# Performance work log

Hardware: AMD Instinct MI355X
Metric: run time of the kernel (lower is better)

Reference implementation:

```python
import jax, jax.numpy as jnp
import numpy as np

B, N, RIN, ROUT, DEMB, FIN, FE, E, ITERS = 64, 128, 32, 64, 64, 64, 16, 65536, 3
NTOT = B * N


def gnn(x, edge_index, edge_feat, Ws, Wm, We, b):
    # edge-conditioned message passing: [NTOT, Fin] -> [NTOT, Fout]
    src, dst = edge_index[0], edge_index[1]
    msg = jax.nn.relu(x[src] @ Wm + edge_feat @ We)          # [E, Fout]
    agg = jax.ops.segment_sum(msg, dst, num_segments=x.shape[0])
    return jax.nn.relu(x @ Ws + agg + b)


def setup_inputs() -> dict:
    key = jax.random.key(0)
    ks = jax.random.split(key, 20)
    s = 0.1
    return {
        "x_r": jax.random.normal(ks[0], (NTOT, FIN), jnp.float32),
        "edge_index_r": jax.random.randint(ks[1], (2, E), 0, NTOT),
        "edge_feat_r": jax.random.normal(ks[2], (E, FE), jnp.float32),
        "x_p": jax.random.normal(ks[3], (NTOT, FIN), jnp.float32),
        "edge_index_p": jax.random.randint(ks[4], (2, E), 0, NTOT),
        "edge_feat_p": jax.random.normal(ks[5], (E, FE), jnp.float32),
        "r_mask": jnp.ones((B, N), dtype=bool),
        "p_mask": jnp.ones((B, N), dtype=bool),
        # gnn_1 params (FIN -> DEMB)
        "g1_Ws": jax.random.normal(ks[6], (FIN, DEMB)) * s,
        "g1_Wm": jax.random.normal(ks[7], (FIN, DEMB)) * s,
        "g1_We": jax.random.normal(ks[8], (FE, DEMB)) * s,
        "g1_b": jnp.zeros((DEMB,), jnp.float32),
        # gnn_2 params (RIN -> ROUT)
        "g2_Ws": jax.random.normal(ks[9], (RIN, ROUT)) * s,
        "g2_Wm": jax.random.normal(ks[10], (RIN, ROUT)) * s,
        "g2_We": jax.random.normal(ks[11], (FE, ROUT)) * s,
        "g2_b": jnp.zeros((ROUT,), jnp.float32),
        # consensus mlp (ROUT -> ROUT -> 1)
        "mlp_W1": jax.random.normal(ks[12], (ROUT, ROUT)) * s,
        "mlp_b1": jnp.zeros((ROUT,), jnp.float32),
        "mlp_W2": jax.random.normal(ks[13], (ROUT, 1)) * s,
        "mlp_b2": jnp.zeros((1,), jnp.float32),
    }


def reference(x_r, edge_index_r, edge_feat_r, x_p, edge_index_p, edge_feat_p,
              r_mask, p_mask,
              g1_Ws, g1_Wm, g1_We, g1_b,
              g2_Ws, g2_Wm, g2_We, g2_b,
              mlp_W1, mlp_b1, mlp_W2, mlp_b2):
    # node embeddings via gnn_1, then dense-batch to [B, N, DEMB]
    h_r = gnn(x_r, edge_index_r, edge_feat_r, g1_Ws, g1_Wm, g1_We, g1_b).reshape(B, N, DEMB)
    h_p = gnn(x_p, edge_index_p, edge_feat_p, g1_Ws, g1_Wm, g1_We, g1_b).reshape(B, N, DEMB)

    M_hat = jnp.einsum('brd,bpd->brp', h_r, h_p)             # [B, N_r, N_p]
    M_mask = r_mask[:, :, None] & p_mask[:, None, :]
    M_0 = jax.nn.softmax(M_hat, axis=-1).reshape(NTOT, N)    # packed (full mask)

    rkey = jax.random.key(42)
    for it in range(ITERS):
        M = jax.nn.softmax(M_hat, axis=-1)
        rf_r = jax.random.normal(jax.random.fold_in(rkey, it), (B, N, RIN), jnp.float32)
        rf_p = jnp.einsum('brp,bri->bpi', M, rf_r)           # M^T @ rand
        o_r = gnn(rf_r.reshape(NTOT, RIN), edge_index_r, edge_feat_r,
                  g2_Ws, g2_Wm, g2_We, g2_b).reshape(B, N, ROUT)
        o_p = gnn(rf_p.reshape(NTOT, RIN), edge_index_p, edge_feat_p,
                  g2_Ws, g2_Wm, g2_We, g2_b).reshape(B, N, ROUT)
        D = o_r[:, :, None, :] - o_p[:, None, :, :]          # [B, N_r, N_p, ROUT]
        upd = (jax.nn.relu(D @ mlp_W1 + mlp_b1) @ mlp_W2 + mlp_b2)[..., 0]
        M_hat = M_hat + jnp.where(M_mask, upd, 0.0)

    M_T = jax.nn.softmax(M_hat, axis=-1).reshape(NTOT, N)
    return (M_0, M_T)
```

## Files before the change

### kernel.cpp

```cpp
#include <hip/hip_runtime.h>

constexpr int kE = 65536, kNTOT = 8192;

__host__ __device__ __forceinline__ void tf_round(unsigned& x0, unsigned& x1, int r) {
  x0 += x1;
  x1 = (x1 << r) | (x1 >> (32 - r));
  x1 ^= x0;
}
__host__ __device__ __forceinline__ void tf2x32(unsigned k0, unsigned k1,
                                                unsigned& x0, unsigned& x1) {
  unsigned ks2 = k0 ^ k1 ^ 0x1BD11BDAu;
  x0 += k0; x1 += k1;
  tf_round(x0,x1,13); tf_round(x0,x1,15); tf_round(x0,x1,26); tf_round(x0,x1,6);
  x0 += k1; x1 += ks2 + 1u;
  tf_round(x0,x1,17); tf_round(x0,x1,29); tf_round(x0,x1,16); tf_round(x0,x1,24);
  x0 += ks2; x1 += k0 + 2u;
  tf_round(x0,x1,13); tf_round(x0,x1,15); tf_round(x0,x1,26); tf_round(x0,x1,6);
  x0 += k0; x1 += k1 + 3u;
  tf_round(x0,x1,17); tf_round(x0,x1,29); tf_round(x0,x1,16); tf_round(x0,x1,24);
  x0 += k1; x1 += ks2 + 4u;
  tf_round(x0,x1,13); tf_round(x0,x1,15); tf_round(x0,x1,26); tf_round(x0,x1,6);
  x0 += ks2; x1 += k0 + 5u;
}

__device__ __forceinline__ float bits_to_normal(unsigned bits) {
  float f = __uint_as_float((bits >> 9) | 0x3f800000u) - 1.0f;
  const float LO = -0.99999994f;
  float u = fmaf(f, 2.0f, LO);
  u = fmaxf(u, LO);
  float w = -log1pf(-u * u);
  float p;
  if (w < 5.0f) {
    w -= 2.5f;
    p = 2.81022636e-08f;
    p = fmaf(p, w, 3.43273939e-07f);
    p = fmaf(p, w, -3.5233877e-06f);
    p = fmaf(p, w, -4.39150654e-06f);
    p = fmaf(p, w, 0.00021858087f);
    p = fmaf(p, w, -0.00125372503f);
    p = fmaf(p, w, -0.00417768164f);
    p = fmaf(p, w, 0.246640727f);
    p = fmaf(p, w, 1.50140941f);
  } else {
    w = sqrtf(w) - 3.0f;
    p = -0.000200214257f;
    p = fmaf(p, w, 0.000100950558f);
    p = fmaf(p, w, 0.00134934322f);
    p = fmaf(p, w, -0.00367342844f);
    p = fmaf(p, w, 0.00573950773f);
    p = fmaf(p, w, -0.0076224613f);
    p = fmaf(p, w, 0.00943887047f);
    p = fmaf(p, w, 1.00167406f);
    p = fmaf(p, w, 2.83297682f);
  }
  return 1.41421356f * (p * u);
}

__device__ __forceinline__ float redmax32(float v) {
#pragma unroll
  for (int o = 16; o > 0; o >>= 1) v = fmaxf(v, __shfl_xor(v, o));
  return v;
}
__device__ __forceinline__ float redsum32(float v) {
#pragma unroll
  for (int o = 16; o > 0; o >>= 1) v += __shfl_xor(v, o);
  return v;
}

__global__ __launch_bounds__(256) void hist_kern(const int* __restrict__ eiR,
                                                 const int* __restrict__ eiP,
                                                 int* __restrict__ offR,
                                                 int* __restrict__ offP,
                                                 float* __restrict__ aggz) {
  int i = blockIdx.x * 256 + threadIdx.x;
  float4 z4 = make_float4(0.f, 0.f, 0.f, 0.f);
  float4* z = reinterpret_cast<float4*>(aggz) + i * 2;
  z[0] = z4; z[1] = z4;
  const int* ei = (i < kE) ? eiR : eiP;
  int* off = (i < kE) ? offR : offP;
  int e = i & (kE - 1);
  atomicAdd(&off[ei[kE + e]], 1);
}

__global__ __launch_bounds__(256) void scan_kern(int* __restrict__ offR,
                                                 int* __restrict__ offP) {
  int* off = blockIdx.x ? offP : offR;
  int t = threadIdx.x;
  int base = t * 32;
  int v[32];
#pragma unroll
  for (int i = 0; i < 32; ++i) v[i] = off[base + i];
  int sum = 0;
#pragma unroll
  for (int i = 0; i < 32; ++i) sum += v[i];
  int lane = t & 63, w = t >> 6;
  int incl = sum;
#pragma unroll
  for (int o = 1; o < 64; o <<= 1) {
    int y = __shfl_up(incl, o);
    if (lane >= o) incl += y;
  }
  __shared__ int wsum[4];
  if (lane == 63) wsum[w] = incl;
  __syncthreads();
  int woff = 0;
#pragma unroll
  for (int i = 0; i < 4; ++i) if (i < w) woff += wsum[i];
  int running = woff + incl - sum;
#pragma unroll
  for (int i = 0; i < 32; ++i) {
    off[base + i] = running;
    running += v[i];
  }
}

__global__ __launch_bounds__(256) void scatter_kern(
    const int* __restrict__ eiR, const int* __restrict__ eiP,
    int* __restrict__ offR, int* __restrict__ offP,
    int* __restrict__ permR, int* __restrict__ permP,
    int* __restrict__ srcsR, int* __restrict__ srcsP,
    int* __restrict__ dstsR, int* __restrict__ dstsP) {
  int i = blockIdx.x * 256 + threadIdx.x;
  const int* ei = (i < kE) ? eiR : eiP;
  int* off = (i < kE) ? offR : offP;
  int* perm = (i < kE) ? permR : permP;
  int* srcs = (i < kE) ? srcsR : srcsP;
  int* dsts = (i < kE) ? dstsR : dstsP;
  int e = i & (kE - 1);
  int dst = ei[kE + e];
  int pos = atomicAdd(&off[dst], 1);
  perm[pos] = e;
  srcs[pos] = ei[e];
  dsts[pos] = dst;
}

template <int KX>
__global__ __launch_bounds__(256) void msg_gemm(
    const float* __restrict__ xR, const float* __restrict__ efR,
    const int* __restrict__ srcsR, const int* __restrict__ permR,
    const int* __restrict__ dstsR, float* __restrict__ aggR,
    const float* __restrict__ xP, const float* __restrict__ efP,
    const int* __restrict__ srcsP, const int* __restrict__ permP,
    const int* __restrict__ dstsP, float* __restrict__ aggP,
    const float* __restrict__ Wm, const float* __restrict__ We,
    const float* __restrict__ We2, float* __restrict__ efweR, float* __restrict__ efweP) {
  constexpr int KT = KX + 16;
  constexpr int SA_ROWS = (KT > 64) ? KT : 64;
  __shared__ float sA[SA_ROWS][68];
  __shared__ float sW[KT][68];
  __shared__ int sDst[64];
// ... 110 lines not shown

__global__ __launch_bounds__(256) void msg_add(
    const float* __restrict__ xwmR, const float* __restrict__ efweR,
    const int* __restrict__ srcsR, const int* __restrict__ dstsR, float* __restrict__ aggR,
    const float* __restrict__ xwmP, const float* __restrict__ efweP,
    const int* __restrict__ srcsP, const int* __restrict__ dstsP, float* __restrict__ aggP) {
  int lane = threadIdx.x & 63;
  int wv = blockIdx.x * 4 + (threadIdx.x >> 6);
  bool isP = wv >= 4096;
  const float* xwm = isP ? xwmP : xwmR;
  const float* efwe = isP ? efweP : efweR;
  const int* srcs = isP ? srcsP : srcsR;
  const int* dsts = isP ? dstsP : dstsR;
  float* agg = isP ? aggP : aggR;
  int e0 = (wv & 4095) * 16;
  float run = 0.f;
  int rd = dsts[e0];
#pragma unroll 4
  for (int k = 0; k < 16; ++k) {
    int e = e0 + k;
    int d = dsts[e];
    if (d != rd) {
      unsafeAtomicAdd(&agg[(size_t)rd * 64 + lane], run);
      run = 0.f; rd = d;
    }
    float v = xwm[(size_t)srcs[e] * 64 + lane] + efwe[(size_t)e * 64 + lane];
    run += fmaxf(v, 0.f);
  }
  unsafeAtomicAdd(&agg[(size_t)rd * 64 + lane], run);
}

__global__ __launch_bounds__(256) void node1_gemm(
    const float* __restrict__ xR, float* __restrict__ aggR, float* __restrict__ hR,
    const float* __restrict__ xP, float* __restrict__ aggP, float* __restrict__ hP,
    const float* __restrict__ Ws, const float* __restrict__ bias) {
  __shared__ float sX[64][68];
  __shared__ float sW[64][68];
  bool isP = blockIdx.x >= 128;
  const float* x = isP ? xP : xR;
  float* agg = isP ? aggP : aggR;
  float* h = isP ? hP : hR;
  int n0 = (blockIdx.x & 127) * 64;
  int t = threadIdx.x;
#pragma unroll
  for (int idx = 0; idx < 4; ++idx) {
    int q = t * 4 + idx * 1024;
    int k = q >> 6, j = q & 63;
    *reinterpret_cast<float4*>(&sW[k][j]) = *reinterpret_cast<const float4*>(Ws + q);
    float4 v = *reinterpret_cast<const float4*>(x + (size_t)n0 * 64 + q);
    sX[j + 0][k] = v.x; sX[j + 1][k] = v.y; sX[j + 2][k] = v.z; sX[j + 3][k] = v.w;
  }
  __syncthreads();
  int tn = (t & 15) * 4, tj = (t >> 4) * 4;
  float acc[4][4] = {};
#pragma unroll 8
  for (int k = 0; k < 64; ++k) {
    float4 a = *reinterpret_cast<const float4*>(&sX[k][tn]);
    float4 b = *reinterpret_cast<const float4*>(&sW[k][tj]);
    acc[0][0] = fmaf(a.x, b.x, acc[0][0]); acc[0][1] = fmaf(a.x, b.y, acc[0][1]);
    acc[0][2] = fmaf(a.x, b.z, acc[0][2]); acc[0][3] = fmaf(a.x, b.w, acc[0][3]);
    acc[1][0] = fmaf(a.y, b.x, acc[1][0]); acc[1][1] = fmaf(a.y, b.y, acc[1][1]);
    acc[1][2] = fmaf(a.y, b.z, acc[1][2]); acc[1][3] = fmaf(a.y, b.w, acc[1][3]);
    acc[2][0] = fmaf(a.z, b.x, acc[2][0]); acc[2][1] = fmaf(a.z, b.y, acc[2][1]);
    acc[2][2] = fmaf(a.z, b.z, acc[2][2]); acc[2][3] = fmaf(a.z, b.w, acc[2][3]);
    acc[3][0] = fmaf(a.w, b.x, acc[3][0]); acc[3][1] = fmaf(a.w, b.y, acc[3][1]);
    acc[3][2] = fmaf(a.w, b.z, acc[3][2]); acc[3][3] = fmaf(a.w, b.w, acc[3][3]);
  }
  float4 bv = *reinterpret_cast<const float4*>(bias + tj);
  float4 z4 = make_float4(0.f, 0.f, 0.f, 0.f);
#pragma unroll
  for (int i = 0; i < 4; ++i) {
    int n = n0 + tn + i;
    float4 g = *reinterpret_cast<const float4*>(&agg[(size_t)n * 64 + tj]);
    *reinterpret_cast<float4*>(&agg[(size_t)n * 64 + tj]) = z4;
    float4 o;
    o.x = fmaxf(acc[i][0] + g.x + bv.x, 0.f);
    o.y = fmaxf(acc[i][1] + g.y + bv.y, 0.f);
    o.z = fmaxf(acc[i][2] + g.z + bv.z, 0.f);
    o.w = fmaxf(acc[i][3] + g.w + bv.w, 0.f);
    *reinterpret_cast<float4*>(&h[(size_t)n * 64 + tj]) = o;
  }
}

__global__ __launch_bounds__(256) void mhat_soft(
    const float* __restrict__ hR, const float* __restrict__ hP,
    float* __restrict__ Mhat, float* __restrict__ Msoft, float* __restrict__ M0out,
    float* __restrict__ rfr, unsigned fk0, unsigned fk1) {
  __shared__ float hr[16][66];
  __shared__ float hp[128][66];
  int gid = blockIdx.x, t = threadIdx.x;
  int gtid = (gid << 8) + t;
#pragma unroll
  for (int q = 0; q < 2; ++q) {
    unsigned i = (unsigned)gtid + (unsigned)q * 131072u;
    unsigned a0 = 0u, a1 = i;
    tf2x32(fk0, fk1, a0, a1);
    rfr[i] = bits_to_normal(a0 ^ a1);
  }
  int b = gid >> 3, r0 = (gid & 7) * 16;
  const float* hrG = hR + ((size_t)(b * 128 + r0)) * 64;
  {
    int q = t * 4; int r = q >> 6, d = q & 63;
    float4 v = *reinterpret_cast<const float4*>(hrG + q);
    hr[r][d] = v.x; hr[r][d + 1] = v.y; hr[r][d + 2] = v.z; hr[r][d + 3] = v.w;
  }
  const float* hpG = hP + (size_t)b * 128 * 64;
#pragma unroll
  for (int rep = 0; rep < 8; ++rep) {
    int q = (rep * 256 + t) * 4; int p = q >> 6, d = q & 63;
    float4 v = *reinterpret_cast<const float4*>(hpG + q);
    hp[p][d] = v.x; hp[p][d + 1] = v.y; hp[p][d + 2] = v.z; hp[p][d + 3] = v.w;
  }
  __syncthreads();
  int tx = t & 31, ty = t >> 5;
  float acc[2][4] = {};
  for (int d = 0; d < 64; ++d) {
    float a0 = hr[ty][d], a1 = hr[ty + 8][d];
    float q0 = hp[tx][d], q1 = hp[tx + 32][d], q2 = hp[tx + 64][d], q3 = hp[tx + 96][d];
    acc[0][0] = fmaf(a0, q0, acc[0][0]); acc[0][1] = fmaf(a0, q1, acc[0][1]);
    acc[0][2] = fmaf(a0, q2, acc[0][2]); acc[0][3] = fmaf(a0, q3, acc[0][3]);
    acc[1][0] = fmaf(a1, q0, acc[1][0]); acc[1][1] = fmaf(a1, q1, acc[1][1]);
    acc[1][2] = fmaf(a1, q2, acc[1][2]); acc[1][3] = fmaf(a1, q3, acc[1][3]);
  }
#pragma unroll
  for (int ii = 0; ii < 2; ++ii) {
    int r = r0 + ty + 8 * ii;
    float* mrow = Mhat + ((size_t)(b * 128 + r)) * 128;
    mrow[tx] = acc[ii][0]; mrow[tx + 32] = acc[ii][1];
    mrow[tx + 64] = acc[ii][2]; mrow[tx + 96] = acc[ii][3];
    float mx = redmax32(fmaxf(fmaxf(acc[ii][0], acc[ii][1]), fmaxf(acc[ii][2], acc[ii][3])));
    float e0 = __expf(acc[ii][0] - mx), e1 = __expf(acc[ii][1] - mx);
    float e2 = __expf(acc[ii][2] - mx), e3 = __expf(acc[ii][3] - mx);
    float inv = 1.0f / redsum32(e0 + e1 + e2 + e3);
    float* srow = Msoft + ((size_t)(b * 128 + r)) * 128;
    srow[tx] = e0 * inv; srow[tx + 32] = e1 * inv;
    srow[tx + 64] = e2 * inv; srow[tx + 96] = e3 * inv;
    float* orow = M0out + ((size_t)(b * 128 + r)) * 128;
    orow[tx] = e0 * inv; orow[tx + 32] = e1 * inv;
    orow[tx + 64] = e2 * inv; orow[tx + 96] = e3 * inv;
  }
}

__global__ __launch_bounds__(256) void rfp_xwm_kern(
    const float* __restrict__ Msoft, const float* __restrict__ rfr,
    float* __restrict__ rfp, const float* __restrict__ Wm2,
    float* __restrict__ xwm_r, float* __restrict__ xwm_p) {
  __shared__ __align__(16) float sm[7232];
  int t = threadIdx.x;
  if (blockIdx.x < 512) {
    float (*rr)[36] = (float(*)[36])sm;
    float (*srow)[36] = (float(*)[36])(sm + 4608);
    float (*swm)[64] = (float(*)[64])(sm + 5184);
    int b = blockIdx.x >> 3, p0 = (blockIdx.x & 7) * 16;
    const float* rfG = rfr + (size_t)b * 4096;
#pragma unroll
    for (int rep = 0; rep < 4; ++rep) {
      int q = (rep * 256 + t) * 4; int r = q >> 5, i = q & 31;
      float4 v = *reinterpret_cast<const float4*>(rfG + q);
      rr[r][i] = v.x; rr[r][i + 1] = v.y; rr[r][i + 2] = v.z; rr[r][i + 3] = v.w;
    }
#pragma unroll
    for (int rep = 0; rep < 2; ++rep) {
      int q = t * 4 + rep * 1024;
      *reinterpret_cast<float4*>(&swm[q >> 6][q & 63]) = *reinterpret_cast<const float4*>(Wm2 + q);
    }
    __syncthreads();
    int pl = t & 15, ih = (t >> 4) * 2;
    int p = p0 + pl;
    const float* Mcol = Msoft + (size_t)b * 16384 + p;
    float a0 = 0.f, a1 = 0.f;
#pragma unroll 8
    for (int r = 0; r < 128; ++r) {
      float m = Mcol[(size_t)r * 128];
      a0 = fmaf(m, rr[r][ih], a0);
      a1 = fmaf(m, rr[r][ih + 1], a1);
    }
    float* dst = rfp + ((size_t)(b * 128 + p)) * 32 + ih;
    dst[0] = a0; dst[1] = a1;
    srow[pl][ih] = a0; srow[pl][ih + 1] = a1;
    __syncthreads();
    int r2 = t & 15, c2 = (t >> 4) * 4;
    float4 av = make_float4(0.f, 0.f, 0.f, 0.f);
#pragma unroll 8
    for (int k = 0; k < 32; ++k) {
      float s = srow[r2][k];
      float4 w = *reinterpret_cast<const float4*>(&swm[k][c2]);
      av.x = fmaf(s, w.x, av.x); av.y = fmaf(s, w.y, av.y);
      av.z = fmaf(s, w.z, av.z); av.w = fmaf(s, w.w, av.w);
    }
    *reinterpret_cast<float4*>(&xwm_p[(size_t)(b * 128 + p0 + r2) * 64 + c2]) = av;
  } else {
    float (*sRF)[68] = (float(*)[68])sm;
    float (*swm)[64] = (float(*)[64])(sm + 2176);
    int n0 = (blockIdx.x - 512) * 64;
#pragma unroll
    for (int rep = 0; rep < 2; ++rep) {
      int q = t * 4 + rep * 1024;
      *reinterpret_cast<float4*>(&swm[q >> 6][q & 63]) = *reinterpret_cast<const float4*>(Wm2 + q);
      int r = q >> 5, kk = q & 31;
      float4 v = *reinterpret_cast<const float4*>(rfr + (size_t)(n0 + r) * 32 + kk);
      sRF[kk][r] = v.x; sRF[kk + 1][r] = v.y; sRF[kk + 2][r] = v.z; sRF[kk + 3][r] = v.w;
    }
    __syncthreads();
    int tn = (t & 15) * 4, tj = (t >> 4) * 4;
    float acc[4][4] = {};
#pragma unroll 8
    for (int k = 0; k < 32; ++k) {
      float4 a = *reinterpret_cast<const float4*>(&sRF[k][tn]);
      float4 b = *reinterpret_cast<const float4*>(&swm[k][tj]);
      acc[0][0] = fmaf(a.x, b.x, acc[0][0]); acc[0][1] = fmaf(a.x, b.y, acc[0][1]);
      acc[0][2] = fmaf(a.x, b.z, acc[0][2]); acc[0][3] = fmaf(a.x, b.w, acc[0][3]);
      acc[1][0] = fmaf(a.y, b.x, acc[1][0]); acc[1][1] = fmaf(a.y, b.y, acc[1][1]);
      acc[1][2] = fmaf(a.y, b.z, acc[1][2]); acc[1][3] = fmaf(a.y, b.w, acc[1][3]);
      acc[2][0] = fmaf(a.z, b.x, acc[2][0]); acc[2][1] = fmaf(a.z, b.y, acc[2][1]);
      acc[2][2] = fmaf(a.z, b.z, acc[2][2]); acc[2][3] = fmaf(a.z, b.w, acc[2][3]);
      acc[3][0] = fmaf(a.w, b.x, acc[3][0]); acc[3][1] = fmaf(a.w, b.y, acc[3][1]);
      acc[3][2] = fmaf(a.w, b.z, acc[3][2]); acc[3][3] = fmaf(a.w, b.w, acc[3][3]);
    }
#pragma unroll
    for (int i = 0; i < 4; ++i) {
      float4 o = make_float4(acc[i][0], acc[i][1], acc[i][2], acc[i][3]);
      *reinterpret_cast<float4*>(&xwm_r[(size_t)(n0 + tn + i) * 64 + tj]) = o;
    }
  }
}

__global__ __launch_bounds__(256) void node2u_gemm(
    const float* __restrict__ rfR, float* __restrict__ aggR, float* __restrict__ uR,
    const float* __restrict__ rfP, float* __restrict__ aggP, float* __restrict__ uP,
    const float* __restrict__ Ws2, const float* __restrict__ g2b,
    const float* __restrict__ W1, const float* __restrict__ b1) {
  __shared__ float sRF[32][68];
  __shared__ float sW2[32][68];
  __shared__ float sW1[64][68];
  __shared__ float sO[64][68];
  bool isP = blockIdx.x >= 128;
  const float* rf = isP ? rfP : rfR;
  float* agg = isP ? aggP : aggR;
  float* u = isP ? uP : uR;
  int n0 = (blockIdx.x & 127) * 64;
  int t = threadIdx.x;
#pragma unroll
  for (int idx = 0; idx < 4; ++idx) {
    int q = t * 4 + idx * 1024;
    *reinterpret_cast<float4*>(&sW1[q >> 6][q & 63]) = *reinterpret_cast<const float4*>(W1 + q);
  }
#pragma unroll
  for (int idx = 0; idx < 2; ++idx) {
    int q = t * 4 + idx * 1024;
    *reinterpret_cast<float4*>(&sW2[q >> 6][q & 63]) = *reinterpret_cast<const float4*>(Ws2 + q);
    int r = q >> 5, kk = q & 31;
    float4 v = *reinterpret_cast<const float4*>(rf + (size_t)(n0 + r) * 32 + kk);
    sRF[kk][r] = v.x; sRF[kk + 1][r] = v.y; sRF[kk + 2][r] = v.z; sRF[kk + 3][r] = v.w;
  }
  __syncthreads();
  int tn = (t & 15) * 4, tj = (t >> 4) * 4;
  float acc[4][4] = {};
#pragma unroll 8
  for (int k = 0; k < 32; ++k) {
    float4 a = *reinterpret_cast<const float4*>(&sRF[k][tn]);
    float4 b = *reinterpret_cast<const float4*>(&sW2[k][tj]);
    acc[0][0] = fmaf(a.x, b.x, acc[0][0]); acc[0][1] = fmaf(a.x, b.y, acc[0][1]);
    acc[0][2] = fmaf(a.x, b.z, acc[0][2]); acc[0][3] = fmaf(a.x, b.w, acc[0][3]);
    acc[1][0] = fmaf(a.y, b.x, acc[1][0]); acc[1][1] = fmaf(a.y, b.y, acc[1][1]);
    acc[1][2] = fmaf(a.y, b.z, acc[1][2]); acc[1][3] = fmaf(a.y, b.w, acc[1][3]);
    acc[2][0] = fmaf(a.z, b.x, acc[2][0]); acc[2][1] = fmaf(a.z, b.y, acc[2][1]);
    acc[2][2] = fmaf(a.z, b.z, acc[2][2]); acc[2][3] = fmaf(a.z, b.w, acc[2][3]);
    acc[3][0] = fmaf(a.w, b.x, acc[3][0]); acc[3][1] = fmaf(a.w, b.y, acc[3][1]);
    acc[3][2] = fmaf(a.w, b.z, acc[3][2]); acc[3][3] = fmaf(a.w, b.w, acc[3][3]);
  }
  float4 bg = *reinterpret_cast<const float4*>(g2b + tj);
  float4 z4 = make_float4(0.f, 0.f, 0.f, 0.f);
#pragma unroll
  for (int i = 0; i < 4; ++i) {
    int n = n0 + tn + i;
    float4 g = *reinterpret_cast<const float4*>(&agg[(size_t)n * 64 + tj]);
    *reinterpret_cast<float4*>(&agg[(size_t)n * 64 + tj]) = z4;
    sO[tj + 0][tn + i] = fmaxf(acc[i][0] + g.x + bg.x, 0.f);
    sO[tj + 1][tn + i] = fmaxf(acc[i][1] + g.y + bg.y, 0.f);
    sO[tj + 2][tn + i] = fmaxf(acc[i][2] + g.z + bg.z, 0.f);
    sO[tj + 3][tn + i] = fmaxf(acc[i][3] + g.w + bg.w, 0.f);
  }
  __syncthreads();
  float acc2[4][4] = {};
#pragma unroll 8
  for (int k = 0; k < 64; ++k) {
    float4 a = *reinterpret_cast<const float4*>(&sO[k][tn]);
    float4 b = *reinterpret_cast<const float4*>(&sW1[k][tj]);
    acc2[0][0] = fmaf(a.x, b.x, acc2[0][0]); acc2[0][1] = fmaf(a.x, b.y, acc2[0][1]);
    acc2[0][2] = fmaf(a.x, b.z, acc2[0][2]); acc2[0][3] = fmaf(a.x, b.w, acc2[0][3]);
    acc2[1][0] = fmaf(a.y, b.x, acc2[1][0]); acc2[1][1] = fmaf(a.y, b.y, acc2[1][1]);
    acc2[1][2] = fmaf(a.y, b.z, acc2[1][2]); acc2[1][3] = fmaf(a.y, b.w, acc2[1][3]);
    acc2[2][0] = fmaf(a.z, b.x, acc2[2][0]); acc2[2][1] = fmaf(a.z, b.y, acc2[2][1]);
    acc2[2][2] = fmaf(a.z, b.z, acc2[2][2]); acc2[2][3] = fmaf(a.z, b.w, acc2[2][3]);
    acc2[3][0] = fmaf(a.w, b.x, acc2[3][0]); acc2[3][1] = fmaf(a.w, b.y, acc2[3][1]);
    acc2[3][2] = fmaf(a.w, b.z, acc2[3][2]); acc2[3][3] = fmaf(a.w, b.w, acc2[3][3]);
  }
  float4 b1v = make_float4(0.f, 0.f, 0.f, 0.f);
  if (!isP) b1v = *reinterpret_cast<const float4*>(b1 + tj);
#pragma unroll
  for (int i = 0; i < 4; ++i) {
    int n = n0 + tn + i;
    float4 o;
    o.x = acc2[i][0] + b1v.x; o.y = acc2[i][1] + b1v.y;
    o.z = acc2[i][2] + b1v.z; o.w = acc2[i][3] + b1v.w;
    *reinterpret_cast<float4*>(&u[(size_t)n * 64 + tj]) = o;
  }
}

__global__ __launch_bounds__(256) void upd_soft(
    const float* __restrict__ uR, const float* __restrict__ uP,
    const float* __restrict__ W2, const float* __restrict__ b2p,
    float* __restrict__ Mhat, float* __restrict__ softDst,
    int writeMhat, float* __restrict__ rfr, int doRng,
    unsigned fk0, unsigned fk1) {
  __shared__ float sur[16][66];
  __shared__ float sup[128][66];
  __shared__ float sw2[64];
  int gid = blockIdx.x, t = threadIdx.x;
  int b = gid >> 3, r0 = (gid & 7) * 16;
  const float* urG = uR + ((size_t)(b * 128 + r0)) * 64;
  {
    int q = t * 4; int r = q >> 6, d = q & 63;
    float4 v = *reinterpret_cast<const float4*>(urG + q);
    sur[r][d] = v.x; sur[r][d + 1] = v.y; sur[r][d + 2] = v.z; sur[r][d + 3] = v.w;
  }
  const float* upG = uP + (size_t)b * 128 * 64;
#pragma unroll
  for (int rep = 0; rep < 8; ++rep) {
    int q = (rep * 256 + t) * 4; int p = q >> 6, d = q & 63;
    float4 v = *reinterpret_cast<const float4*>(upG + q);
    sup[p][d] = v.x; sup[p][d + 1] = v.y; sup[p][d + 2] = v.z; sup[p][d + 3] = v.w;
  }
  if (t < 64) sw2[t] = W2[t];
  __syncthreads();
  int tx = t & 31, ty = t >> 5;
  float acc[2][4] = {};
  for (int j = 0; j < 64; ++j) {
    float w2v = sw2[j];
    float a0 = sur[ty][j], a1 = sur[ty + 8][j];
    float q0 = sup[tx][j], q1 = sup[tx + 32][j], q2 = sup[tx + 64][j], q3 = sup[tx + 96][j];
    acc[0][0] = fmaf(fmaxf(a0 - q0, 0.f), w2v, acc[0][0]);
    acc[0][1] = fmaf(fmaxf(a0 - q1, 0.f), w2v, acc[0][1]);
    acc[0][2] = fmaf(fmaxf(a0 - q2, 0.f), w2v, acc[0][2]);
    acc[0][3] = fmaf(fmaxf(a0 - q3, 0.f), w2v, acc[0][3]);
    acc[1][0] = fmaf(fmaxf(a1 - q0, 0.f), w2v, acc[1][0]);
    acc[1][1] = fmaf(fmaxf(a1 - q1, 0.f), w2v, acc[1][1]);
    acc[1][2] = fmaf(fmaxf(a1 - q2, 0.f), w2v, acc[1][2]);
    acc[1][3] = fmaf(fmaxf(a1 - q3, 0.f), w2v, acc[1][3]);
  }
  float b2v = b2p[0];
#pragma unroll
  for (int ii = 0; ii < 2; ++ii) {
    int r = r0 + ty + 8 * ii;
    float* mrow = Mhat + ((size_t)(b * 128 + r)) * 128;
    float m0 = mrow[tx] + acc[ii][0] + b2v;
    float m1 = mrow[tx + 32] + acc[ii][1] + b2v;
    float m2 = mrow[tx + 64] + acc[ii][2] + b2v;
    float m3 = mrow[tx + 96] + acc[ii][3] + b2v;
    if (writeMhat) {
      mrow[tx] = m0; mrow[tx + 32] = m1; mrow[tx + 64] = m2; mrow[tx + 96] = m3;
    }
    float mx = redmax32(fmaxf(fmaxf(m0, m1), fmaxf(m2, m3)));
    float e0 = __expf(m0 - mx), e1 = __expf(m1 - mx);
    float e2 = __expf(m2 - mx), e3 = __expf(m3 - mx);
    float inv = 1.0f / redsum32(e0 + e1 + e2 + e3);
    float* srow = softDst + ((size_t)(b * 128 + r)) * 128;
    srow[tx] = e0 * inv; srow[tx + 32] = e1 * inv;
    srow[tx + 64] = e2 * inv; srow[tx + 96] = e3 * inv;
  }
  if (doRng) {
    int gtid = (gid << 8) + t;
#pragma unroll
    for (int q = 0; q < 2; ++q) {
      unsigned i = (unsigned)gtid + (unsigned)q * 131072u;
      unsigned a0 = 0u, a1 = i;
      tf2x32(fk0, fk1, a0, a1);
      rfr[i] = bits_to_normal(a0 ^ a1);
    }
  }
}

extern "C" void kernel_launch(void* const* d_in, const int* in_sizes, int n_in,
                              void* d_out, int out_size, void* d_ws, size_t ws_size,
                              hipStream_t stream) {
  (void)in_sizes; (void)n_in; (void)out_size; (void)ws_size;
  const float* x_r  = (const float*)d_in[0];
  const int*   ei_r = (const int*)d_in[1];
  const float* ef_r = (const float*)d_in[2];
  const float* x_p  = (const float*)d_in[3];
  const int*   ei_p = (const int*)d_in[4];
  const float* ef_p = (const float*)d_in[5];
  const float* g1_Ws = (const float*)d_in[8];
  const float* g1_Wm = (const float*)d_in[9];
  const float* g1_We = (const float*)d_in[10];
  const float* g1_b  = (const float*)d_in[11];
  const float* g2_Ws = (const float*)d_in[12];
  const float* g2_Wm = (const float*)d_in[13];
  const float* g2_We = (const float*)d_in[14];
  const float* g2_b  = (const float*)d_in[15];
  const float* W1 = (const float*)d_in[16];
  const float* b1 = (const float*)d_in[17];
  const float* W2 = (const float*)d_in[18];
  const float* b2 = (const float*)d_in[19];
  float* out = (float*)d_out;

  float* ws = (float*)d_ws;
  float* h_r   = ws;
  float* h_p   = h_r + 524288;
  float* Mhat  = h_p + 524288;
  float* Msoft = Mhat + 1048576;
  float* rfr   = Msoft + 1048576;
  float* rfp   = rfr + 262144;
  float* u_r   = rfp + 262144;
  float* u_p   = u_r + 524288;
  float* agg_r = u_p + 524288;
  float* agg_p = agg_r + 524288;
  float* efwe_r = agg_p + 524288;
  float* efwe_p = efwe_r + 4194304;
  int* ib      = (int*)(efwe_p + 4194304);
  int* off_r  = ib;
  int* off_p  = off_r + 8192;
  int* perm_r = off_p + 8192;
  int* perm_p = perm_r + 65536;
  int* srcs_r = perm_p + 65536;
  int* srcs_p = srcs_r + 65536;
  int* dsts_r = srcs_p + 65536;
  int* dsts_p = dsts_r + 65536;
  float* xwm_r = u_r;
  float* xwm_p = u_p;

  unsigned fk0[3], fk1[3];
  for (int it = 0; it < 3; ++it) {
    unsigned a = 0u, c = (unsigned)it;
    tf2x32(0u, 42u, a, c);
    fk0[it] = a; fk1[it] = c;
  }

  hipMemsetAsync(off_r, 0, 2 * 8192 * sizeof(int), stream);
  hist_kern<<<512, 256, 0, stream>>>(ei_r, ei_p, off_r, off_p, agg_r);
  scan_kern<<<2, 256, 0, stream>>>(off_r, off_p);
  scatter_kern<<<512, 256, 0, stream>>>(ei_r, ei_p, off_r, off_p,
                                        perm_r, perm_p, srcs_r, srcs_p,
                                        dsts_r, dsts_p);

  msg_gemm<64><<<4096, 256, 0, stream>>>(x_r, ef_r, srcs_r, perm_r, dsts_r, agg_r,
                                         x_p, ef_p, srcs_p, perm_p, dsts_p, agg_p,
                                         g1_Wm, g1_We, g2_We, efwe_r, efwe_p);
  node1_gemm<<<256, 256, 0, stream>>>(x_r, agg_r, h_r, x_p, agg_p, h_p, g1_Ws, g1_b);
  mhat_soft<<<512, 256, 0, stream>>>(h_r, h_p, Mhat, Msoft, out, rfr, fk0[0], fk1[0]);

  for (int it = 0; it < 3; ++it) {
    rfp_xwm_kern<<<640, 256, 0, stream>>>(Msoft, rfr, rfp, g2_Wm, xwm_r, xwm_p);
    msg_add<<<2048, 256, 0, stream>>>(xwm_r, efwe_r, srcs_r, dsts_r, agg_r,
                                      xwm_p, efwe_p, srcs_p, dsts_p, agg_p);
    node2u_gemm<<<256, 256, 0, stream>>>(rfr, agg_r, u_r, rfp, agg_p, u_p,
                                         g2_Ws, g2_b, W1, b1);
    int last = (it == 2);
    upd_soft<<<512, 256, 0, stream>>>(u_r, u_p, W2, b2, Mhat,
                                      last ? (out + 1048576) : Msoft,
                                      !last,
                                      rfr, !last,
                                      fk0[it < 2 ? it + 1 : 0], fk1[it < 2 ? it + 1 : 0]);
  }
}
```

Measured before the change: 320.2 us.

## Fuse softmax, RNG, M^T·rand and Wm projection into per-batch fat kernels

Replaces the row-tiled mhat_soft/upd_soft kernels and the separate rfp_xwm kernel with per-batch kernels (one block per graph) that keep the whole 128x128 softmax matrix in LDS, generate the random features, compute M^T·rand and both Wm2 projections in the same launch. This removes the Msoft round-trip through global memory and one launch per iteration, and uses 8x8 register tiles for the pairwise stage. In exchange the grid shrinks to 64 blocks with about 110 KB of dynamic LDS each, so most of the GPU's compute units sit idle and there is little latency hiding. Dynamic LDS above 64 KB may also need an explicit attribute to launch.

```diff
diff --git a/kernel.cpp b/kernel.cpp
--- a/kernel.cpp
+++ b/kernel.cpp
@@ -1,6 +1,7 @@
 #include <hip/hip_runtime.h>
 
 constexpr int kE = 65536, kNTOT = 8192;
+constexpr int FAT_LDS_BYTES = 110080;
 
 __host__ __device__ __forceinline__ void tf_round(unsigned& x0, unsigned& x1, int r) {
   x0 += x1;
@@ -56,16 +57,22 @@
   return 1.41421356f * (p * u);
 }
 
-__device__ __forceinline__ float redmax32(float v) {
-#pragma unroll
-  for (int o = 16; o > 0; o >>= 1) v = fmaxf(v, __shfl_xor(v, o));
+__device__ __forceinline__ float redmax16(float v) {
+#pragma unroll
+  for (int o = 1; o < 16; o <<= 1) v = fmaxf(v, __shfl_xor(v, o));
   return v;
 }
-__device__ __forceinline__ float redsum32(float v) {
-#pragma unroll
-  for (int o = 16; o > 0; o >>= 1) v += __shfl_xor(v, o);
+__device__ __forceinline__ float redsum16(float v) {
+#pragma unroll
+  for (int o = 1; o < 16; o <<= 1) v += __shfl_xor(v, o);
   return v;
 }
+
+constexpr int O_M = 0;
+constexpr int O_RR = 16896;
+constexpr int O_RFP = 21120;
+constexpr int O_WM2 = 25344;
+constexpr int O_W2 = 27392;
 
 __global__ __launch_bounds__(256) void hist_kern(const int* __restrict__ eiR,
                                                  const int* __restrict__ eiP,
@@ -342,149 +349,6 @@
   }
 }
 
-__global__ __launch_bounds__(256) void mhat_soft(
-    const float* __restrict__ hR, const float* __restrict__ hP,
-    float* __restrict__ Mhat, float* __restrict__ Msoft, float* __restrict__ M0out,
-    float* __restrict__ rfr, unsigned fk0, unsigned fk1) {
-  __shared__ float hr[16][66];
-  __shared__ float hp[128][66];
-  int gid = blockIdx.x, t = threadIdx.x;
-  int gtid = (gid << 8) + t;
-#pragma unroll
-  for (int q = 0; q < 2; ++q) {
-    unsigned i = (unsigned)gtid + (unsigned)q * 131072u;
-    unsigned a0 = 0u, a1 = i;
-    tf2x32(fk0, fk1, a0, a1);
-    rfr[i] = bits_to_normal(a0 ^ a1);
-  }
-  int b = gid >> 3, r0 = (gid & 7) * 16;
-  const float* hrG = hR + ((size_t)(b * 128 + r0)) * 64;
-  {
-    int q = t * 4; int r = q >> 6, d = q & 63;
-    float4 v = *reinterpret_cast<const float4*>(hrG + q);
-    hr[r][d] = v.x; hr[r][d + 1] = v.y; hr[r][d + 2] = v.z; hr[r][d + 3] = v.w;
-  }
-  const float* hpG = hP + (size_t)b * 128 * 64;
-#pragma unroll
-  for (int rep = 0; rep < 8; ++rep) {
-    int q = (rep * 256 + t) * 4; int p = q >> 6, d = q & 63;
-    float4 v = *reinterpret_cast<const float4*>(hpG + q);
-    hp[p][d] = v.x; hp[p][d + 1] = v.y; hp[p][d + 2] = v.z; hp[p][d + 3] = v.w;
-  }
-  __syncthreads();
-  int tx = t & 31, ty = t >> 5;
-  float acc[2][4] = {};
-  for (int d = 0; d < 64; ++d) {
-    float a0 = hr[ty][d], a1 = hr[ty + 8][d];
-    float q0 = hp[tx][d], q1 = hp[tx + 32][d], q2 = hp[tx + 64][d], q3 = hp[tx + 96][d];
-    acc[0][0] = fmaf(a0, q0, acc[0][0]); acc[0][1] = fmaf(a0, q1, acc[0][1]);
-    acc[0][2] = fmaf(a0, q2, acc[0][2]); acc[0][3] = fmaf(a0, q3, acc[0][3]);
-    acc[1][0] = fmaf(a1, q0, acc[1][0]); acc[1][1] = fmaf(a1, q1, acc[1][1]);
-    acc[1][2] = fmaf(a1, q2, acc[1][2]); acc[1][3] = fmaf(a1, q3, acc[1][3]);
-  }
-#pragma unroll
-  for (int ii = 0; ii < 2; ++ii) {
-    int r = r0 + ty + 8 * ii;
-    float* mrow = Mhat + ((size_t)(b * 128 + r)) * 128;
-    mrow[tx] = acc[ii][0]; mrow[tx + 32] = acc[ii][1];
-    mrow[tx + 64] = acc[ii][2]; mrow[tx + 96] = acc[ii][3];
-    float mx = redmax32(fmaxf(fmaxf(acc[ii][0], acc[ii][1]), fmaxf(acc[ii][2], acc[ii][3])));
-    float e0 = __expf(acc[ii][0] - mx), e1 = __expf(acc[ii][1] - mx);
-    float e2 = __expf(acc[ii][2] - mx), e3 = __expf(acc[ii][3] - mx);
-    float inv = 1.0f / redsum32(e0 + e1 + e2 + e3);
-    float* srow = Msoft + ((size_t)(b * 128 + r)) * 128;
-    srow[tx] = e0 * inv; srow[tx + 32] = e1 * inv;
-    srow[tx + 64] = e2 * inv; srow[tx + 96] = e3 * inv;
-    float* orow = M0out + ((size_t)(b * 128 + r)) * 128;
-    orow[tx] = e0 * inv; orow[tx + 32] = e1 * inv;
-    orow[tx + 64] = e2 * inv; orow[tx + 96] = e3 * inv;
-  }
-}
-
-__global__ __launch_bounds__(256) void rfp_xwm_kern(
-    const float* __restrict__ Msoft, const float* __restrict__ rfr,
-    float* __restrict__ rfp, const float* __restrict__ Wm2,
-    float* __restrict__ xwm_r, float* __restrict__ xwm_p) {
-  __shared__ __align__(16) float sm[7232];
-  int t = threadIdx.x;
-  if (blockIdx.x < 512) {
-    float (*rr)[36] = (float(*)[36])sm;
-    float (*srow)[36] = (float(*)[36])(sm + 4608);
-    float (*swm)[64] = (float(*)[64])(sm + 5184);
-    int b = blockIdx.x >> 3, p0 = (blockIdx.x & 7) * 16;
-    const float* rfG = rfr + (size_t)b * 4096;
-#pragma unroll
-    for (int rep = 0; rep < 4; ++rep) {
-      int q = (rep * 256 + t) * 4; int r = q >> 5, i = q & 31;
-      float4 v = *reinterpret_cast<const float4*>(rfG + q);
-      rr[r][i] = v.x; rr[r][i + 1] = v.y; rr[r][i + 2] = v.z; rr[r][i + 3] = v.w;
-    }
-#pragma unroll
-    for (int rep = 0; rep < 2; ++rep) {
-      int q = t * 4 + rep * 1024;
-      *reinterpret_cast<float4*>(&swm[q >> 6][q & 63]) = *reinterpret_cast<const float4*>(Wm2 + q);
-    }
-    __syncthreads();
-    int pl = t & 15, ih = (t >> 4) * 2;
-    int p = p0 + pl;
-    const float* Mcol = Msoft + (size_t)b * 16384 + p;
-    float a0 = 0.f, a1 = 0.f;
-#pragma unroll 8
-    for (int r = 0; r < 128; ++r) {
-      float m = Mcol[(size_t)r * 128];
-      a0 = fmaf(m, rr[r][ih], a0);
-      a1 = fmaf(m, rr[r][ih + 1], a1);
-    }
-    float* dst = rfp + ((size_t)(b * 128 + p)) * 32 + ih;
-    dst[0] = a0; dst[1] = a1;
-    srow[pl][ih] = a0; srow[pl][ih + 1] = a1;
-    __syncthreads();
-    int r2 = t & 15, c2 = (t >> 4) * 4;
-    float4 av = make_float4(0.f, 0.f, 0.f, 0.f);
-#pragma unroll 8
-    for (int k = 0; k < 32; ++k) {
-      float s = srow[r2][k];
-      float4 w = *reinterpret_cast<const float4*>(&swm[k][c2]);
-      av.x = fmaf(s, w.x, av.x); av.y = fmaf(s, w.y, av.y);
-      av.z = fmaf(s, w.z, av.z); av.w = fmaf(s, w.w, av.w);
-    }
-    *reinterpret_cast<float4*>(&xwm_p[(size_t)(b * 128 + p0 + r2) * 64 + c2]) = av;
-  } else {
-    float (*sRF)[68] = (float(*)[68])sm;
-    float (*swm)[64] = (float(*)[64])(sm + 2176);
-    int n0 = (blockIdx.x - 512) * 64;
-#pragma unroll
-    for (int rep = 0; rep < 2; ++rep) {
-      int q = t * 4 + rep * 1024;
-      *reinterpret_cast<float4*>(&swm[q >> 6][q & 63]) = *reinterpret_cast<const float4*>(Wm2 + q);
-      int r = q >> 5, kk = q & 31;
-      float4 v = *reinterpret_cast<const float4*>(rfr + (size_t)(n0 + r) * 32 + kk);
-      sRF[kk][r] = v.x; sRF[kk + 1][r] = v.y; sRF[kk + 2][r] = v.z; sRF[kk + 3][r] = v.w;
-    }
-    __syncthreads();
-    int tn = (t & 15) * 4, tj = (t >> 4) * 4;
-    float acc[4][4] = {};
-#pragma unroll 8
-    for (int k = 0; k < 32; ++k) {
-      float4 a = *reinterpret_cast<const float4*>(&sRF[k][tn]);
-      float4 b = *reinterpret_cast<const float4*>(&swm[k][tj]);
-      acc[0][0] = fmaf(a.x, b.x, acc[0][0]); acc[0][1] = fmaf(a.x, b.y, acc[0][1]);
-      acc[0][2] = fmaf(a.x, b.z, acc[0][2]); acc[0][3] = fmaf(a.x, b.w, acc[0][3]);
-      acc[1][0] = fmaf(a.y, b.x, acc[1][0]); acc[1][1] = fmaf(a.y, b.y, acc[1][1]);
-      acc[1][2] = fmaf(a.y, b.z, acc[1][2]); acc[1][3] = fmaf(a.y, b.w, acc[1][3]);
-      acc[2][0] = fmaf(a.z, b.x, acc[2][0]); acc[2][1] = fmaf(a.z, b.y, acc[2][1]);
-      acc[2][2] = fmaf(a.z, b.z, acc[2][2]); acc[2][3] = fmaf(a.z, b.w, acc[2][3]);
-      acc[3][0] = fmaf(a.w, b.x, acc[3][0]); acc[3][1] = fmaf(a.w, b.y, acc[3][1]);
-      acc[3][2] = fmaf(a.w, b.z, acc[3][2]); acc[3][3] = fmaf(a.w, b.w, acc[3][3]);
-    }
-#pragma unroll
-    for (int i = 0; i < 4; ++i) {
-      float4 o = make_float4(acc[i][0], acc[i][1], acc[i][2], acc[i][3]);
-      *reinterpret_cast<float4*>(&xwm_r[(size_t)(n0 + tn + i) * 64 + tj]) = o;
-    }
-  }
-}
-
 __global__ __launch_bounds__(256) void node2u_gemm(
     const float* __restrict__ rfR, float* __restrict__ aggR, float* __restrict__ uR,
     const float* __restrict__ rfP, float* __restrict__ aggP, float* __restrict__ uP,
@@ -568,77 +432,220 @@
   }
 }
 
-__global__ __launch_bounds__(256) void upd_soft(
+__device__ __forceinline__ void fat_tail(float* sm, int b, int t,
+    float* __restrict__ rfr, float* __restrict__ rfp,
+    float* __restrict__ xwm_r, float* __restrict__ xwm_p,
+    unsigned fk0, unsigned fk1) {
+#pragma unroll
+  for (int q = 0; q < 16; ++q) {
+    int il = q * 256 + t;
+    unsigned i = (unsigned)(b * 4096 + il);
+    unsigned a0 = 0u, a1 = i;
+    tf2x32(fk0, fk1, a0, a1);
+    float nv = bits_to_normal(a0 ^ a1);
+    sm[O_RR + (il >> 5) * 33 + (il & 31)] = nv;
+    rfr[b * 4096 + il] = nv;
+  }
+  __syncthreads();
+  int p = t >> 1, hf = t & 1;
+  float acc[16] = {};
+  for (int r = 0; r < 128; ++r) {
+    float m = sm[O_M + r * 132 + p];
+    const float* rrr = &sm[O_RR + r * 33 + hf * 16];
+#pragma unroll
+    for (int i = 0; i < 16; ++i) acc[i] = fmaf(m, rrr[i], acc[i]);
+  }
+  float* dst = rfp + ((size_t)(b * 128 + p)) * 32 + hf * 16;
+#pragma unroll
+  for (int i = 0; i < 16; i += 4)
+    *reinterpret_cast<float4*>(dst + i) = make_float4(acc[i], acc[i+1], acc[i+2], acc[i+3]);
+#pragma unroll
+  for (int i = 0; i < 16; ++i) sm[O_RFP + p * 33 + hf * 16 + i] = acc[i];
+  __syncthreads();
+  int ch = (t & 1) * 32;
+  float4 ap[8] = {}, ar[8] = {};
+  for (int k = 0; k < 32; ++k) {
+    float sp = sm[O_RFP + p * 33 + k];
+    float sr = sm[O_RR + p * 33 + k];
+    const float* wrow = &sm[O_WM2 + k * 64 + ch];
+#pragma unroll
+    for (int c = 0; c < 8; ++c) {
+      float4 w = *reinterpret_cast<const float4*>(wrow + c * 4);
+      ap[c].x = fmaf(sp, w.x, ap[c].x); ap[c].y = fmaf(sp, w.y, ap[c].y);
+      ap[c].z = fmaf(sp, w.z, ap[c].z); ap[c].w = fmaf(sp, w.w, ap[c].w);
+      ar[c].x = fmaf(sr, w.x, ar[c].x); ar[c].y = fmaf(sr, w.y, ar[c].y);
+      ar[c].z = fmaf(sr, w.z, ar[c].z); ar[c].w = fmaf(sr, w.w, ar[c].w);
+    }
+  }
+  float* xp = xwm_p + ((size_t)(b * 128 + p)) * 64 + ch;
+  float* xr = xwm_r + ((size_t)(b * 128 + p)) * 64 + ch;
+#pragma unroll
+  for (int c = 0; c < 8; ++c) {
+    *reinterpret_cast<float4*>(xp + c * 4) = ap[c];
+    *reinterpret_cast<float4*>(xr + c * 4) = ar[c];
+  }
+}
+
+__device__ __forceinline__ void stage_T(float* sm, int off, const float* __restrict__ g,
+                                        int b, int t) {
+  const float* gp = g + (size_t)b * 128 * 64;
+#pragma unroll
+  for (int rep = 0; rep < 8; ++rep) {
+    int q = (rep * 256 + t) * 4;
+    int n = q >> 6, d = q & 63;
+    float4 v = *reinterpret_cast<const float4*>(gp + q);
+    sm[off + (d + 0) * 132 + n] = v.x;
+    sm[off + (d + 1) * 132 + n] = v.y;
+    sm[off + (d + 2) * 132 + n] = v.z;
+    sm[off + (d + 3) * 132 + n] = v.w;
+  }
+}
+
+__global__ __launch_bounds__(256) void mhat_fat(
+    const float* __restrict__ hR, const float* __restrict__ hP,
+    float* __restrict__ Mhat, float* __restrict__ M0out,
+    float* __restrict__ rfr, float* __restrict__ rfp,
+    float* __restrict__ xwm_r, float* __restrict__ xwm_p,
+    const float* __restrict__ Wm2, unsigned fk0, unsigned fk1) {
+  extern __shared__ float sm[];
+  int b = blockIdx.x, t = threadIdx.x;
+#pragma unroll
+  for (int rep = 0; rep < 2; ++rep) {
+    int q = t * 4 + rep * 1024;
+    *reinterpret_cast<float4*>(&sm[O_WM2 + q]) = *reinterpret_cast<const float4*>(Wm2 + q);
+  }
+  stage_T(sm, 0, hR, b, t);
+  stage_T(sm, 8448, hP, b, t);
+  __syncthreads();
+  int tx = t & 15, ty = t >> 4;
+  float acc[8][8] = {};
+  for (int d = 0; d < 64; ++d) {
+    const float* ra = &sm[d * 132 + ty * 8];
+    const float* rq = &sm[8448 + d * 132 + tx * 8];
+    float4 a0 = *reinterpret_cast<const float4*>(ra);
+    float4 a1 = *reinterpret_cast<const float4*>(ra + 4);
+    float4 q0 = *reinterpret_cast<const float4*>(rq);
+    float4 q1 = *reinterpret_cast<const float4*>(rq + 4);
+    float av[8] = {a0.x,a0.y,a0.z,a0.w,a1.x,a1.y,a1.z,a1.w};
+    float qv[8] = {q0.x,q0.y,q0.z,q0.w,q1.x,q1.y,q1.z,q1.w};
+#pragma unroll
+    for (int i = 0; i < 8; ++i)
+#pragma unroll
+      for (int k = 0; k < 8; ++k) acc[i][k] = fmaf(av[i], qv[k], acc[i][k]);
+  }
+  float prob[8][8];
+#pragma unroll
+  for (int i = 0; i < 8; ++i) {
+    int r = ty * 8 + i;
+    float* mrow = Mhat + ((size_t)(b * 128 + r)) * 128 + tx * 8;
+    *reinterpret_cast<float4*>(mrow) = make_float4(acc[i][0], acc[i][1], acc[i][2], acc[i][3]);
+    *reinterpret_cast<float4*>(mrow + 4) = make_float4(acc[i][4], acc[i][5], acc[i][6], acc[i][7]);
+    float mx = acc[i][0];
+#pragma unroll
+    for (int k = 1; k < 8; ++k) mx = fmaxf(mx, acc[i][k]);
+    mx = redmax16(mx);
+    float s = 0.f;
+#pragma unroll
+    for (int k = 0; k < 8; ++k) { prob[i][k] = __expf(acc[i][k] - mx); s += prob[i][k]; }
+    s = redsum16(s);
+    float inv = 1.0f / s;
+    float* orow = M0out + ((size_t)(b * 128 + r)) * 128 + tx * 8;
+#pragma unroll
+    for (int k = 0; k < 8; ++k) prob[i][k] *= inv;
+    *reinterpret_cast<float4*>(orow) = make_float4(prob[i][0], prob[i][1], prob[i][2], prob[i][3]);
+    *reinterpret_cast<float4*>(orow + 4) = make_float4(prob[i][4], prob[i][5], prob[i][6], prob[i][7]);
+  }
+  __syncthreads();
+#pragma unroll
+  for (int i = 0; i < 8; ++i) {
+    int r = ty * 8 + i;
+#pragma unroll
+    for (int k = 0; k < 8; ++k) sm[O_M + r * 132 + tx * 8 + k] = prob[i][k];
+  }
+  __syncthreads();
+  fat_tail(sm, b, t, rfr, rfp, xwm_r, xwm_p, fk0, fk1);
+}
+
+__global__ __launch_bounds__(256) void upd_fat(
     const float* __restrict__ uR, const float* __restrict__ uP,
     const float* __restrict__ W2, const float* __restrict__ b2p,
-    float* __restrict__ Mhat, float* __restrict__ softDst,
-    int writeMhat, float* __restrict__ rfr, int doRng,
-    unsigned fk0, unsigned fk1) {
-  __shared__ float sur[16][66];
-  __shared__ float sup[128][66];
-  __shared__ float sw2[64];
-  int gid = blockIdx.x, t = threadIdx.x;
-  int b = gid >> 3, r0 = (gid & 7) * 16;
-  const float* urG = uR + ((size_t)(b * 128 + r0)) * 64;
-  {
-    int q = t * 4; int r = q >> 6, d = q & 63;
-    float4 v = *reinterpret_cast<const float4*>(urG + q);
-    sur[r][d] = v.x; sur[r][d + 1] = v.y; sur[r][d + 2] = v.z; sur[r][d + 3] = v.w;
-  }
-  const float* upG = uP + (size_t)b * 128 * 64;
-#pragma unroll
-  for (int rep = 0; rep < 8; ++rep) {
-    int q = (rep * 256 + t) * 4; int p = q >> 6, d = q & 63;
-    float4 v = *reinterpret_cast<const float4*>(upG + q);
-    sup[p][d] = v.x; sup[p][d + 1] = v.y; sup[p][d + 2] = v.z; sup[p][d + 3] = v.w;
-  }
-  if (t < 64) sw2[t] = W2[t];
-  __syncthreads();
-  int tx = t & 31, ty = t >> 5;
-  float acc[2][4] = {};
+    float* __restrict__ Mhat, float* __restrict__ outLast, int last,
+    float* __restrict__ rfr, float* __restrict__ rfp,
+    float* __restrict__ xwm_r, float* __restrict__ xwm_p,
+    const float* __restrict__ Wm2, unsigned fk0, unsigned fk1) {
+  extern __shared__ float sm[];
+  int b = blockIdx.x, t = threadIdx.x;
+  if (!last) {
+#pragma unroll
+    for (int rep = 0; rep < 2; ++rep) {
+      int q = t * 4 + rep * 1024;
+      *reinterpret_cast<float4*>(&sm[O_WM2 + q]) = *reinterpret_cast<const float4*>(Wm2 + q);
+    }
+  }
+  if (t < 64) sm[O_W2 + t] = W2[t];
+  stage_T(sm, 0, uR, b, t);
+  stage_T(sm, 8448, uP, b, t);
+  __syncthreads();
+  int tx = t & 15, ty = t >> 4;
+  float acc[8][8] = {};
   for (int j = 0; j < 64; ++j) {
-    float w2v = sw2[j];
-    float a0 = sur[ty][j], a1 = sur[ty + 8][j];
-    float q0 = sup[tx][j], q1 = sup[tx + 32][j], q2 = sup[tx + 64][j], q3 = sup[tx + 96][j];
-    acc[0][0] = fmaf(fmaxf(a0 - q0, 0.f), w2v, acc[0][0]);
-    acc[0][1] = fmaf(fmaxf(a0 - q1, 0.f), w2v, acc[0][1]);
-    acc[0][2] = fmaf(fmaxf(a0 - q2, 0.f), w2v, acc[0][2]);
-    acc[0][3] = fmaf(fmaxf(a0 - q3, 0.f), w2v, acc[0][3]);
-    acc[1][0] = fmaf(fmaxf(a1 - q0, 0.f), w2v, acc[1][0]);
-    acc[1][1] = fmaf(fmaxf(a1 - q1, 0.f), w2v, acc[1][1]);
-    acc[1][2] = fmaf(fmaxf(a1 - q2, 0.f), w2v, acc[1][2]);
-    acc[1][3] = fmaf(fmaxf(a1 - q3, 0.f), w2v, acc[1][3]);
+    float w2v = sm[O_W2 + j];
+    const float* ra = &sm[j * 132 + ty * 8];
+    const float* rq = &sm[8448 + j * 132 + tx * 8];
+    float4 a0 = *reinterpret_cast<const float4*>(ra);
+    float4 a1 = *reinterpret_cast<const float4*>(ra + 4);
+    float4 q0 = *reinterpret_cast<const float4*>(rq);
+    float4 q1 = *reinterpret_cast<const float4*>(rq + 4);
+    float av[8] = {a0.x,a0.y,a0.z,a0.w,a1.x,a1.y,a1.z,a1.w};
+    float qv[8] = {q0.x,q0.y,q0.z,q0.w,q1.x,q1.y,q1.z,q1.w};
+#pragma unroll
+    for (int i = 0; i < 8; ++i)
+#pragma unroll
+      for (int k = 0; k < 8; ++k)
+        acc[i][k] = fmaf(fmaxf(av[i] - qv[k], 0.f), w2v, acc[i][k]);
   }
   float b2v = b2p[0];
-#pragma unroll
-  for (int ii = 0; ii < 2; ++ii) {
-    int r = r0 + ty + 8 * ii;
-    float* mrow = Mhat + ((size_t)(b * 128 + r)) * 128;
-    float m0 = mrow[tx] + acc[ii][0] + b2v;
-    float m1 = mrow[tx + 32] + acc[ii][1] + b2v;
-    float m2 = mrow[tx + 64] + acc[ii][2] + b2v;
-    float m3 = mrow[tx + 96] + acc[ii][3] + b2v;
-    if (writeMhat) {
-      mrow[tx] = m0; mrow[tx + 32] = m1; mrow[tx + 64] = m2; mrow[tx + 96] = m3;
-    }
-    float mx = redmax32(fmaxf(fmaxf(m0, m1), fmaxf(m2, m3)));
-    float e0 = __expf(m0 - mx), e1 = __expf(m1 - mx);
-    float e2 = __expf(m2 - mx), e3 = __expf(m3 - mx);
-    float inv = 1.0f / redsum32(e0 + e1 + e2 + e3);
-    float* srow = softDst + ((size_t)(b * 128 + r)) * 128;
-    srow[tx] = e0 * inv; srow[tx + 32] = e1 * inv;
-    srow[tx + 64] = e2 * inv; srow[tx + 96] = e3 * inv;
-  }
-  if (doRng) {
-    int gtid = (gid << 8) + t;
-#pragma unroll
-    for (int q = 0; q < 2; ++q) {
-      unsigned i = (unsigned)gtid + (unsigned)q * 131072u;
-      unsigned a0 = 0u, a1 = i;
-      tf2x32(fk0, fk1, a0, a1);
-      rfr[i] = bits_to_normal(a0 ^ a1);
-    }
-  }
+  float prob[8][8];
+#pragma unroll
+  for (int i = 0; i < 8; ++i) {
+    int r = ty * 8 + i;
+    float* mrow = Mhat + ((size_t)(b * 128 + r)) * 128 + tx * 8;
+    float4 g0 = *reinterpret_cast<const float4*>(mrow);
+    float4 g1 = *reinterpret_cast<const float4*>(mrow + 4);
+    float m[8] = {g0.x,g0.y,g0.z,g0.w,g1.x,g1.y,g1.z,g1.w};
+#pragma unroll
+    for (int k = 0; k < 8; ++k) m[k] += acc[i][k] + b2v;
+    if (!last) {
+      *reinterpret_cast<float4*>(mrow) = make_float4(m[0], m[1], m[2], m[3]);
+      *reinterpret_cast<float4*>(mrow + 4) = make_float4(m[4], m[5], m[6], m[7]);
+    }
+    float mx = m[0];
+#pragma unroll
+    for (int k = 1; k < 8; ++k) mx = fmaxf(mx, m[k]);
+    mx = redmax16(mx);
+    float s = 0.f;
+#pragma unroll
+    for (int k = 0; k < 8; ++k) { prob[i][k] = __expf(m[k] - mx); s += prob[i][k]; }
+    s = redsum16(s);
+    float inv = 1.0f / s;
+#pragma unroll
+    for (int k = 0; k < 8; ++k) prob[i][k] *= inv;
+    if (last) {
+      float* orow = outLast + ((size_t)(b * 128 + r)) * 128 + tx * 8;
+      *reinterpret_cast<float4*>(orow) = make_float4(prob[i][0], prob[i][1], prob[i][2], prob[i][3]);
+      *reinterpret_cast<float4*>(orow + 4) = make_float4(prob[i][4], prob[i][5], prob[i][6], prob[i][7]);
+    }
+  }
+  if (last) return;
+  __syncthreads();
+#pragma unroll
+  for (int i = 0; i < 8; ++i) {
+    int r = ty * 8 + i;
+#pragma unroll
+    for (int k = 0; k < 8; ++k) sm[O_M + r * 132 + tx * 8 + k] = prob[i][k];
+  }
+  __syncthreads();
+  fat_tail(sm, b, t, rfr, rfp, xwm_r, xwm_p, fk0, fk1);
 }
 
 extern "C" void kernel_launch(void* const* d_in, const int* in_sizes, int n_in,
@@ -669,8 +676,7 @@
   float* h_r   = ws;
   float* h_p   = h_r + 524288;
   float* Mhat  = h_p + 524288;
-  float* Msoft = Mhat + 1048576;
-  float* rfr   = Msoft + 1048576;
+  float* rfr   = Mhat + 1048576;
   float* rfp   = rfr + 262144;
   float* u_r   = rfp + 262144;
   float* u_p   = u_r + 524288;
@@ -708,19 +714,19 @@
                                          x_p, ef_p, srcs_p, perm_p, dsts_p, agg_p,
                                          g1_Wm, g1_We, g2_We, efwe_r, efwe_p);
   node1_gemm<<<256, 256, 0, stream>>>(x_r, agg_r, h_r, x_p, agg_p, h_p, g1_Ws, g1_b);
-  mhat_soft<<<512, 256, 0, stream>>>(h_r, h_p, Mhat, Msoft, out, rfr, fk0[0], fk1[0]);
+  mhat_fat<<<64, 256, FAT_LDS_BYTES, stream>>>(h_r, h_p, Mhat, out, rfr, rfp,
+                                               xwm_r, xwm_p, g2_Wm, fk0[0], fk1[0]);
 
   for (int it = 0; it < 3; ++it) {
-    rfp_xwm_kern<<<640, 256, 0, stream>>>(Msoft, rfr, rfp, g2_Wm, xwm_r, xwm_p);
     msg_add<<<2048, 256, 0, stream>>>(xwm_r, efwe_r, srcs_r, dsts_r, agg_r,
                                       xwm_p, efwe_p, srcs_p, dsts_p, agg_p);
     node2u_gemm<<<256, 256, 0, stream>>>(rfr, agg_r, u_r, rfp, agg_p, u_p,
                                          g2_Ws, g2_b, W1, b1);
     int last = (it == 2);
-    upd_soft<<<512, 256, 0, stream>>>(u_r, u_p, W2, b2, Mhat,
-                                      last ? (out + 1048576) : Msoft,
-                                      !last,
-                                      rfr, !last,
-                                      fk0[it < 2 ? it + 1 : 0], fk1[it < 2 ? it + 1 : 0]);
-  }
-}
+    upd_fat<<<64, 256, FAT_LDS_BYTES, stream>>>(u_r, u_p, W2, b2, Mhat,
+                                                out + 1048576, last,
+                                                rfr, rfp, xwm_r, xwm_p, g2_Wm,
+                                                fk0[last ? 0 : it + 1],
+                                                fk1[last ? 0 : it + 1]);
+  }
+}
```

Measured after the change: 542.2 us. +69.3%, slower.
